# Kernel optimization log

Hardware: AMD Instinct MI355X
Metric: run time of the kernel (lower is better)

## Reference

```python
import jax, jax.numpy as jnp
import numpy as np

B, N, D, H, K = 8, 128, 256, 128, 8

def setup_inputs() -> dict:
    key = jax.random.key(0)
    ks = jax.random.split(key, 6)
    E = jax.random.normal(ks[0], (B, N, D), dtype=jnp.float32)
    # kaiming_uniform-like init for linear weights
    lim1 = np.sqrt(6.0 / (2 * D))
    W1 = jax.random.uniform(ks[1], (H, 2 * D), minval=-lim1, maxval=lim1, dtype=jnp.float32)
    b1 = jnp.zeros((H,), dtype=jnp.float32)
    lim2 = np.sqrt(6.0 / H)
    W2 = jax.random.uniform(ks[2], (D, H), minval=-lim2, maxval=lim2, dtype=jnp.float32)
    b2 = jnp.zeros((D,), dtype=jnp.float32)
    q = jax.random.normal(ks[3], (K, D), dtype=jnp.float32) * (1.0 / D ** 0.5)
    return {"E": E, "W1": W1, "b1": b1, "W2": W2, "b2": b2, "q": q}

def reference(E, W1, b1, W2, b2, q):
    # phi(cat(Ei,Ej)) == relu(E_i @ W1a^T + E_j @ W1b^T + b1) @ W2^T + b2
    # Split first linear's weight to avoid materializing the [B,N,N,2D] concat.
    W1a, W1b = W1[:, :D], W1[:, D:]          # each [H, D]
    Ai = jnp.einsum('bnd,hd->bnh', E, W1a)   # [B,N,H] (row half)
    Aj = jnp.einsum('bnd,hd->bnh', E, W1b)   # [B,N,H] (col half)
    hidden = jax.nn.relu(Ai[:, :, None, :] + Aj[:, None, :, :] + b1)  # [B,N,N,H]
    # dropout is identity at inference
    # Fuse second linear with query dot: (hidden @ W2^T + b2) . q_h
    #   = hidden @ (W2^T q_h) + b2.q_h
    Wq = jnp.einsum('dh,kd->hk', W2, q)      # [H, K]
    bq = jnp.einsum('d,kd->k', b2, q)        # [K]
    logits = jnp.einsum('bijh,hk->bijh'[:0] or 'bijh,hk->bijk', hidden, Wq) + bq  # [B,N,N,K]
    M = jax.nn.sigmoid(logits).transpose(0, 3, 1, 2)  # [B,K,N,N]
    eye = jnp.eye(N, dtype=M.dtype)[None, None]
    return M * (1.0 - eye)
```

## Files before the change

### kernel.cpp

```cpp
#include <hip/hip_runtime.h>

#define PB 8
#define PN 128
#define PD 256
#define PH 128
#define PK 8
#define D2 (2*PD)
#define NT 4

__global__ __launch_bounds__(256, 2) void k1_proj(
        const float* __restrict__ E,  const float* __restrict__ W1,
        const float* __restrict__ b1, const float* __restrict__ W2,
        const float* __restrict__ b2, const float* __restrict__ q,
        float* __restrict__ Ai, float* __restrict__ Ajt,
        float* __restrict__ Wq, float* __restrict__ bq)
{
    const int blk = blockIdx.x, t = threadIdx.x;

    if (blk < 512) {
        __shared__ float es[NT][PD];
        __shared__ float wtile[64][PH + 1];
        const int b    = blk >> 6;
        const int rest = blk & 63;
        const int n0   = (rest >> 1) * NT;
        const int part = rest & 1;
        const int h    = t & (PH - 1);
        const int s    = t >> 7;

        const float* erow = E + (b * PN + n0) * PD;
        float* esf = &es[0][0];
        #pragma unroll
        for (int r = 0; r < 4; ++r) esf[r * 256 + t] = erow[r * 256 + t];

        const int na = n0 + 2 * s;
        float acca = 0.f, accb = 0.f;
        const float* w1row = W1 + h * D2 + part * PD;

        for (int dc = 0; dc < 4; ++dc) {
            __syncthreads();
            const int cb = dc * 64 + s * 32;
            #pragma unroll
            for (int qq = 0; qq < 8; ++qq) {
                float4 v = *reinterpret_cast<const float4*>(w1row + cb + qq * 4);
                const int ld = s * 32 + qq * 4;
                wtile[ld + 0][h] = v.x;
                wtile[ld + 1][h] = v.y;
                wtile[ld + 2][h] = v.z;
                wtile[ld + 3][h] = v.w;
            }
            __syncthreads();
            const int dbase = dc * 64;
            #pragma unroll
            for (int g = 0; g < 16; ++g) {
                const float w0  = wtile[g * 4 + 0][h];
                const float w1v = wtile[g * 4 + 1][h];
                const float w2v = wtile[g * 4 + 2][h];
                const float w3v = wtile[g * 4 + 3][h];
                float4 ea = *reinterpret_cast<const float4*>(&es[2 * s + 0][dbase + g * 4]);
                float4 eb = *reinterpret_cast<const float4*>(&es[2 * s + 1][dbase + g * 4]);
                acca = fmaf(w0, ea.x, acca); acca = fmaf(w1v, ea.y, acca);
                acca = fmaf(w2v, ea.z, acca); acca = fmaf(w3v, ea.w, acca);
                accb = fmaf(w0, eb.x, accb); accb = fmaf(w1v, eb.y, accb);
                accb = fmaf(w2v, eb.z, accb); accb = fmaf(w3v, eb.w, accb);
            }
        }

        if (part == 0) {
            const float bb = b1[h];
            Ai[(b * PN + na) * PH + h]     = acca + bb;
            Ai[(b * PN + na + 1) * PH + h] = accb + bb;
        } else {
            *reinterpret_cast<float2*>(&Ajt[(b * PH + h) * PN + na]) =
                make_float2(acca, accb);
        }
    } else {
        __shared__ float qs[PD];
        __shared__ float red[256];
        const int k = blk - 512;
        qs[t] = q[k * PD + t];
        __syncthreads();
        if (t < PH) {
            float acc = 0.f;
            #pragma unroll 4
            for (int d = 0; d < PD; ++d)
                acc = fmaf(W2[d * PH + t], qs[d], acc);
            Wq[t * PK + k] = acc;
        }
        red[t] = b2[t] * qs[t];
        __syncthreads();
        for (int st = 128; st > 0; st >>= 1) {
            if (t < st) red[t] += red[t + st];
            __syncthreads();
        }
        if (t == 0) bq[k] = red[0];
    }
}

__global__ __launch_bounds__(256) void k2_score(
        const float* __restrict__ Ai, const float* __restrict__ Ajt,
        const float* __restrict__ Wq, const float* __restrict__ bq,
        float* __restrict__ out)
{
    __shared__ float wqh[PH * 4];
    __shared__ float ais[2 * PH];
    __shared__ float bqs[4];

    const int blk = blockIdx.x, t = threadIdx.x;
    const int b  = blk >> 7;
    const int r  = blk & 127;
    const int i0 = (r >> 1) << 1;
    const int kh = r & 1;

    if (t < PH)
        *reinterpret_cast<float4*>(&wqh[t * 4]) =
            *reinterpret_cast<const float4*>(&Wq[t * PK + 4 * kh]);
    ais[t] = Ai[(b * PN + i0) * PH + t];
    if (t < 4) bqs[t] = bq[4 * kh + t];
    __syncthreads();

    const int half = t >> 7;
    const int i = i0 + half;
    const int j = t & (PN - 1);
    const float* ail = ais + half * PH;
    const float* aj = Ajt + b * PH * PN + j;

    float acc[4];
    #pragma unroll
    for (int k = 0; k < 4; ++k) acc[k] = bqs[k];

    #pragma unroll 8
    for (int h = 0; h < PH; ++h) {
        const float v = fmaxf(ail[h] + aj[h * PN], 0.f);
        float4 w0 = *reinterpret_cast<const float4*>(&wqh[h * 4]);
        acc[0] = fmaf(v, w0.x, acc[0]); acc[1] = fmaf(v, w0.y, acc[1]);
        acc[2] = fmaf(v, w0.z, acc[2]); acc[3] = fmaf(v, w0.w, acc[3]);
    }

    #pragma unroll
    for (int k = 0; k < 4; ++k) {
        float s = 1.f / (1.f + __expf(-acc[k]));
        if (j == i) s = 0.f;
        out[((b * PK + 4 * kh + k) * PN + i) * PN + j] = s;
    }
}

extern "C" void kernel_launch(void* const* d_in, const int* in_sizes, int n_in,
                              void* d_out, int out_size, void* d_ws, size_t ws_size,
                              hipStream_t stream) {
    const float* E  = (const float*)d_in[0];
    const float* W1 = (const float*)d_in[1];
    const float* b1 = (const float*)d_in[2];
    const float* W2 = (const float*)d_in[3];
    const float* b2 = (const float*)d_in[4];
    const float* q  = (const float*)d_in[5];

    float* Ai  = (float*)d_ws;
    float* Ajt = Ai + PB * PN * PH;
    float* Wq  = Ajt + PB * PN * PH;
    float* bq  = Wq + PH * PK;

    k1_proj<<<520, 256, 0, stream>>>(E, W1, b1, W2, b2, q, Ai, Ajt, Wq, bq);
    k2_score<<<PB * PN, 256, 0, stream>>>(Ai, Ajt, Wq, bq, (float*)d_out);
}
```

Baseline: 97.38 us.

## Pre-transpose W1 and increase per-thread register tiling in projection and score kernels

Adds a prep kernel that transposes W1 into a float4 layout indexed by d-quad and h, so the projection kernel reads weights straight from global memory, coalesced, with no shared-memory staging or extra barriers. The projection kernel now computes four rows per thread. The score kernel computes all eight K outputs for two j columns per thread, so each relu value is reused across all K and the grid shrinks from 1024 to 256 blocks. The cost is an extra launch, more registers per thread, and fewer blocks, which lowers parallelism on a GPU with many CUs.

```diff
diff --git a/kernel.cpp b/kernel.cpp
--- a/kernel.cpp
+++ b/kernel.cpp
@@ -6,77 +6,30 @@
 #define PH 128
 #define PK 8
 #define D2 (2*PD)
-#define NT 4
 
-__global__ __launch_bounds__(256, 2) void k1_proj(
-        const float* __restrict__ E,  const float* __restrict__ W1,
-        const float* __restrict__ b1, const float* __restrict__ W2,
+__global__ __launch_bounds__(256) void k0_prep(
+        const float* __restrict__ W1, const float* __restrict__ W2,
         const float* __restrict__ b2, const float* __restrict__ q,
-        float* __restrict__ Ai, float* __restrict__ Ajt,
-        float* __restrict__ Wq, float* __restrict__ bq)
+        float4* __restrict__ W1t4, float* __restrict__ Wq, float* __restrict__ bq)
 {
     const int blk = blockIdx.x, t = threadIdx.x;
-
-    if (blk < 512) {
-        __shared__ float es[NT][PD];
-        __shared__ float wtile[64][PH + 1];
-        const int b    = blk >> 6;
-        const int rest = blk & 63;
-        const int n0   = (rest >> 1) * NT;
-        const int part = rest & 1;
-        const int h    = t & (PH - 1);
-        const int s    = t >> 7;
-
-        const float* erow = E + (b * PN + n0) * PD;
-        float* esf = &es[0][0];
+    if (blk < 64) {
+        __shared__ float sm[32][33];
+        const int h0 = (blk >> 4) * 32;
+        const int d0 = (blk & 15) * 32;
+        const int tx = t & 31, ty = t >> 5;
         #pragma unroll
-        for (int r = 0; r < 4; ++r) esf[r * 256 + t] = erow[r * 256 + t];
-
-        const int na = n0 + 2 * s;
-        float acca = 0.f, accb = 0.f;
-        const float* w1row = W1 + h * D2 + part * PD;
-
-        for (int dc = 0; dc < 4; ++dc) {
-            __syncthreads();
-            const int cb = dc * 64 + s * 32;
-            #pragma unroll
-            for (int qq = 0; qq < 8; ++qq) {
-                float4 v = *reinterpret_cast<const float4*>(w1row + cb + qq * 4);
-                const int ld = s * 32 + qq * 4;
-                wtile[ld + 0][h] = v.x;
-                wtile[ld + 1][h] = v.y;
-                wtile[ld + 2][h] = v.z;
-                wtile[ld + 3][h] = v.w;
-            }
-            __syncthreads();
-            const int dbase = dc * 64;
-            #pragma unroll
-            for (int g = 0; g < 16; ++g) {
-                const float w0  = wtile[g * 4 + 0][h];
-                const float w1v = wtile[g * 4 + 1][h];
-                const float w2v = wtile[g * 4 + 2][h];
-                const float w3v = wtile[g * 4 + 3][h];
-                float4 ea = *reinterpret_cast<const float4*>(&es[2 * s + 0][dbase + g * 4]);
-                float4 eb = *reinterpret_cast<const float4*>(&es[2 * s + 1][dbase + g * 4]);
-                acca = fmaf(w0, ea.x, acca); acca = fmaf(w1v, ea.y, acca);
-                acca = fmaf(w2v, ea.z, acca); acca = fmaf(w3v, ea.w, acca);
-                accb = fmaf(w0, eb.x, accb); accb = fmaf(w1v, eb.y, accb);
-                accb = fmaf(w2v, eb.z, accb); accb = fmaf(w3v, eb.w, accb);
-            }
-        }
-
-        if (part == 0) {
-            const float bb = b1[h];
-            Ai[(b * PN + na) * PH + h]     = acca + bb;
-            Ai[(b * PN + na + 1) * PH + h] = accb + bb;
-        } else {
-            *reinterpret_cast<float2*>(&Ajt[(b * PH + h) * PN + na]) =
-                make_float2(acca, accb);
-        }
+        for (int r = 0; r < 4; ++r)
+            sm[ty + 8 * r][tx] = W1[(h0 + ty + 8 * r) * D2 + d0 + tx];
+        __syncthreads();
+        const int hl = t & 31, dql = t >> 5;
+        float4 w = make_float4(sm[hl][dql * 4 + 0], sm[hl][dql * 4 + 1],
+                               sm[hl][dql * 4 + 2], sm[hl][dql * 4 + 3]);
+        W1t4[((d0 >> 2) + dql) * PH + h0 + hl] = w;
     } else {
         __shared__ float qs[PD];
         __shared__ float red[256];
-        const int k = blk - 512;
+        const int k = blk - 64;
         qs[t] = q[k * PD + t];
         __syncthreads();
         if (t < PH) {
@@ -96,51 +49,119 @@
     }
 }
 
+__global__ __launch_bounds__(256) void k1_proj(
+        const float* __restrict__ E, const float* __restrict__ b1,
+        const float4* __restrict__ W1t4,
+        float* __restrict__ Ai, float* __restrict__ Ajt)
+{
+    __shared__ float es[8 * PD];
+    const int blk = blockIdx.x, t = threadIdx.x;
+    const int b    = blk >> 5;
+    const int part = (blk >> 4) & 1;
+    const int ng   = blk & 15;
+    const int h    = t & (PH - 1);
+    const int s    = t >> 7;
+
+    const float* eb = E + (b * PN + ng * 8) * PD;
+    #pragma unroll
+    for (int r = 0; r < 8; ++r) es[r * PD + t] = eb[r * PD + t];
+    __syncthreads();
+
+    const float4* wp = W1t4 + (part * 64) * PH + h;
+    const float* e0 = es + (s * 4 + 0) * PD;
+    const float* e1 = e0 + PD;
+    const float* e2 = e1 + PD;
+    const float* e3 = e2 + PD;
+
+    float a0 = 0.f, a1 = 0.f, a2 = 0.f, a3 = 0.f;
+    #pragma unroll 4
+    for (int dq = 0; dq < 64; ++dq) {
+        const float4 w  = wp[dq * PH];
+        const float4 p0 = *reinterpret_cast<const float4*>(e0 + dq * 4);
+        const float4 p1 = *reinterpret_cast<const float4*>(e1 + dq * 4);
+        const float4 p2 = *reinterpret_cast<const float4*>(e2 + dq * 4);
+        const float4 p3 = *reinterpret_cast<const float4*>(e3 + dq * 4);
+        a0 = fmaf(w.x, p0.x, a0); a0 = fmaf(w.y, p0.y, a0);
+        a0 = fmaf(w.z, p0.z, a0); a0 = fmaf(w.w, p0.w, a0);
+        a1 = fmaf(w.x, p1.x, a1); a1 = fmaf(w.y, p1.y, a1);
+        a1 = fmaf(w.z, p1.z, a1); a1 = fmaf(w.w, p1.w, a1);
+        a2 = fmaf(w.x, p2.x, a2); a2 = fmaf(w.y, p2.y, a2);
+        a2 = fmaf(w.z, p2.z, a2); a2 = fmaf(w.w, p2.w, a2);
+        a3 = fmaf(w.x, p3.x, a3); a3 = fmaf(w.y, p3.y, a3);
+        a3 = fmaf(w.z, p3.z, a3); a3 = fmaf(w.w, p3.w, a3);
+    }
+
+    const int n0 = ng * 8 + s * 4;
+    if (part == 0) {
+        const float bb = b1[h];
+        Ai[(b * PN + n0 + 0) * PH + h] = a0 + bb;
+        Ai[(b * PN + n0 + 1) * PH + h] = a1 + bb;
+        Ai[(b * PN + n0 + 2) * PH + h] = a2 + bb;
+        Ai[(b * PN + n0 + 3) * PH + h] = a3 + bb;
+    } else {
+        *reinterpret_cast<float4*>(&Ajt[(b * PH + h) * PN + n0]) =
+            make_float4(a0, a1, a2, a3);
+    }
+}
+
 __global__ __launch_bounds__(256) void k2_score(
         const float* __restrict__ Ai, const float* __restrict__ Ajt,
         const float* __restrict__ Wq, const float* __restrict__ bq,
         float* __restrict__ out)
 {
-    __shared__ float wqh[PH * 4];
-    __shared__ float ais[2 * PH];
-    __shared__ float bqs[4];
+    __shared__ float  ais[4 * PH];
+    __shared__ float4 wqs[2 * PH];
+    __shared__ float  bqs[PK];
 
     const int blk = blockIdx.x, t = threadIdx.x;
-    const int b  = blk >> 7;
-    const int r  = blk & 127;
-    const int i0 = (r >> 1) << 1;
-    const int kh = r & 1;
+    const int b  = blk >> 5;
+    const int ig = blk & 31;
+    const int i0 = ig * 4;
+    const int il = t >> 6;
+    const int jb = t & 63;
 
-    if (t < PH)
-        *reinterpret_cast<float4*>(&wqh[t * 4]) =
-            *reinterpret_cast<const float4*>(&Wq[t * PK + 4 * kh]);
-    ais[t] = Ai[(b * PN + i0) * PH + t];
-    if (t < 4) bqs[t] = bq[4 * kh + t];
+    ais[t]       = Ai[(b * PN + i0) * PH + t];
+    ais[256 + t] = Ai[(b * PN + i0) * PH + 256 + t];
+    wqs[t] = reinterpret_cast<const float4*>(Wq)[t];
+    if (t < PK) bqs[t] = bq[t];
     __syncthreads();
 
-    const int half = t >> 7;
-    const int i = i0 + half;
-    const int j = t & (PN - 1);
-    const float* ail = ais + half * PH;
-    const float* aj = Ajt + b * PH * PN + j;
+    const float* ail = ais + il * PH;
+    const float* ajr = Ajt + b * PH * PN + jb;
 
-    float acc[4];
+    float acc0[PK], acc1[PK];
     #pragma unroll
-    for (int k = 0; k < 4; ++k) acc[k] = bqs[k];
+    for (int k = 0; k < PK; ++k) { acc0[k] = bqs[k]; acc1[k] = bqs[k]; }
 
-    #pragma unroll 8
-    for (int h = 0; h < PH; ++h) {
-        const float v = fmaxf(ail[h] + aj[h * PN], 0.f);
-        float4 w0 = *reinterpret_cast<const float4*>(&wqh[h * 4]);
-        acc[0] = fmaf(v, w0.x, acc[0]); acc[1] = fmaf(v, w0.y, acc[1]);
-        acc[2] = fmaf(v, w0.z, acc[2]); acc[3] = fmaf(v, w0.w, acc[3]);
+    #pragma unroll 4
+    for (int hh = 0; hh < PH; ++hh) {
+        const float a  = ail[hh];
+        const float g0 = ajr[hh * PN];
+        const float g1 = ajr[hh * PN + 64];
+        const float v0 = fmaxf(a + g0, 0.f);
+        const float v1 = fmaxf(a + g1, 0.f);
+        const float4 wA = wqs[hh * 2];
+        const float4 wB = wqs[hh * 2 + 1];
+        acc0[0] = fmaf(v0, wA.x, acc0[0]); acc0[1] = fmaf(v0, wA.y, acc0[1]);
+        acc0[2] = fmaf(v0, wA.z, acc0[2]); acc0[3] = fmaf(v0, wA.w, acc0[3]);
+        acc0[4] = fmaf(v0, wB.x, acc0[4]); acc0[5] = fmaf(v0, wB.y, acc0[5]);
+        acc0[6] = fmaf(v0, wB.z, acc0[6]); acc0[7] = fmaf(v0, wB.w, acc0[7]);
+        acc1[0] = fmaf(v1, wA.x, acc1[0]); acc1[1] = fmaf(v1, wA.y, acc1[1]);
+        acc1[2] = fmaf(v1, wA.z, acc1[2]); acc1[3] = fmaf(v1, wA.w, acc1[3]);
+        acc1[4] = fmaf(v1, wB.x, acc1[4]); acc1[5] = fmaf(v1, wB.y, acc1[5]);
+        acc1[6] = fmaf(v1, wB.z, acc1[6]); acc1[7] = fmaf(v1, wB.w, acc1[7]);
     }
 
+    const int i = i0 + il;
     #pragma unroll
-    for (int k = 0; k < 4; ++k) {
-        float s = 1.f / (1.f + __expf(-acc[k]));
-        if (j == i) s = 0.f;
-        out[((b * PK + 4 * kh + k) * PN + i) * PN + j] = s;
+    for (int k = 0; k < PK; ++k) {
+        float s0 = 1.f / (1.f + __expf(-acc0[k]));
+        float s1 = 1.f / (1.f + __expf(-acc1[k]));
+        if (jb == i)      s0 = 0.f;
+        if (jb + 64 == i) s1 = 0.f;
+        float* orow = out + ((b * PK + k) * PN + i) * PN;
+        orow[jb]      = s0;
+        orow[jb + 64] = s1;
     }
 }
 
@@ -154,11 +175,13 @@
     const float* b2 = (const float*)d_in[4];
     const float* q  = (const float*)d_in[5];
 
-    float* Ai  = (float*)d_ws;
-    float* Ajt = Ai + PB * PN * PH;
-    float* Wq  = Ajt + PB * PN * PH;
-    float* bq  = Wq + PH * PK;
+    float*  Ai   = (float*)d_ws;
+    float*  Ajt  = Ai + PB * PN * PH;
+    float4* W1t4 = (float4*)(Ajt + PB * PH * PN);
+    float*  Wq   = (float*)(W1t4 + 128 * PH);
+    float*  bq   = Wq + PH * PK;
 
-    k1_proj<<<520, 256, 0, stream>>>(E, W1, b1, W2, b2, q, Ai, Ajt, Wq, bq);
-    k2_score<<<PB * PN, 256, 0, stream>>>(Ai, Ajt, Wq, bq, (float*)d_out);
+    k0_prep<<<72,  256, 0, stream>>>(W1, W2, b2, q, W1t4, Wq, bq);
+    k1_proj<<<256, 256, 0, stream>>>(E, b1, W1t4, Ai, Ajt);
+    k2_score<<<256, 256, 0, stream>>>(Ai, Ajt, Wq, bq, (float*)d_out);
 }
```

Measured after the change: 103.8 us. +6.6%, slower.
